# Optimization experiments

Measured on AMD Instinct MI355X. Metric: run time of the kernel, lower is better.

The kernel has to match this reference:

```python
import jax, jax.numpy as jnp
import numpy as np

H = 64  # hidden_size
B, T1, T2, T3 = 4096, 512, 256, 128


def setup_inputs() -> dict:
    key = jax.random.key(0)
    ks = jax.random.split(key, 18)
    s = 1.0 / np.sqrt(H)  # torch LSTMCell init scale
    def p(k, shape, scale):
        return jax.random.normal(k, shape, dtype=jnp.float32) * scale
    return {
        "x1": p(ks[0], (B, T1), 1.0),
        "x2": p(ks[1], (B, T2), 1.0),
        "x3": p(ks[2], (B, T3), 1.0),
        "W_ih3": p(ks[3], (4 * H, 3), s), "W_hh3": p(ks[4], (4 * H, H), s),
        "b_ih3": p(ks[5], (4 * H,), s), "b_hh3": p(ks[6], (4 * H,), s),
        "W_ih2": p(ks[7], (4 * H, 2), s), "W_hh2": p(ks[8], (4 * H, H), s),
        "b_ih2": p(ks[9], (4 * H,), s), "b_hh2": p(ks[10], (4 * H,), s),
        "W_ih1": p(ks[11], (4 * H, 1), s), "W_hh1": p(ks[12], (4 * H, H), s),
        "b_ih1": p(ks[13], (4 * H,), s), "b_hh1": p(ks[14], (4 * H,), s),
        "W_out": p(ks[15], (1, H), s), "b_out": p(ks[16], (1,), s),
    }


def reference(x1, x2, x3,
              W_ih3, W_hh3, b_ih3, b_hh3,
              W_ih2, W_hh2, b_ih2, b_hh2,
              W_ih1, W_hh1, b_ih1, b_hh1,
              W_out, b_out):
    h = W_hh3.shape[1]
    Bb, t1 = x1.shape
    r2, r3 = t1 // x2.shape[1], t1 // x3.shape[1]
    # Pad input weights to width 3; concat order is [x1, x2, x3] (zeros where absent),
    # so padded-column zeros reproduce the narrower cells exactly.
    Wi = jnp.stack([W_ih3,
                    jnp.pad(W_ih2, ((0, 0), (0, 1))),
                    jnp.pad(W_ih1, ((0, 0), (0, 2)))])  # [3, 4H, 3]
    Wh = jnp.stack([W_hh3, W_hh2, W_hh1])               # [3, 4H, H]
    bs = jnp.stack([b_ih3 + b_hh3, b_ih2 + b_hh2, b_ih1 + b_hh1])  # [3, 4H]
    t = np.arange(t1)
    has2 = (t % r2 == 0)
    has3 = (t % r3 == 0)
    assert not np.any(has3 & ~has2), "ratio2 must divide ratio3 for the concat-order mapping"
    # width 3 -> cell3 (type 0), width 2 -> cell2 (type 1), width 1 -> cell1 (type 2)
    step_type = jnp.asarray(2 - has2.astype(np.int32) - has3.astype(np.int32))
    xs = jnp.zeros((t1, Bb, 3), x1.dtype)
    xs = xs.at[:, :, 0].set(x1.T)
    xs = xs.at[::r2, :, 1].set(x2.T)
    xs = xs.at[::r3, :, 2].set(x3.T)

    def step(carry, inp):
        hx, cx = carry
        x, ty = inp
        g = x @ Wi[ty].T + hx @ Wh[ty].T + bs[ty]  # [B, 4H]
        i, f, gg, o = jnp.split(g, 4, axis=-1)     # torch gate order i,f,g,o
        cx = jax.nn.sigmoid(f) * cx + jax.nn.sigmoid(i) * jnp.tanh(gg)
        hx = jax.nn.sigmoid(o) * jnp.tanh(cx)
        return (hx, cx), None

    z = jnp.zeros((Bb, h), x1.dtype)
    (hx, _), _ = jax.lax.scan(step, (z, z), (xs, step_type))
    return jax.nn.sigmoid(hx @ W_out.T + b_out)  # [B, 1]
```

## Files before the change

### kernel.cpp

```cpp
#include <hip/hip_runtime.h>


typedef __attribute__((ext_vector_type(8))) short short8v;
typedef __attribute__((ext_vector_type(4))) float float4v;
typedef __attribute__((ext_vector_type(4))) unsigned short ushort4v;
typedef __attribute__((ext_vector_type(2))) unsigned int uint2v;

template <int N> struct IC { static constexpr int value = N; };

#define AST 72
#define XS1 516
#define XS2 260
#define XS3 132

#if __has_builtin(__builtin_amdgcn_exp2f)
#define EXP2F(x) __builtin_amdgcn_exp2f(x)
#else
#define EXP2F(x) exp2f(x)
#endif
#if __has_builtin(__builtin_amdgcn_rcpf)
#define RCPF(x) __builtin_amdgcn_rcpf(x)
#else
#define RCPF(x) (1.0f / (x))
#endif

#define NL2E -1.4426950408889634f
#define NL2E2 -2.8853900817779268f

__device__ __forceinline__ short f2bf(float f) {
  union { float f; unsigned u; } v; v.f = f;
  unsigned r = v.u + 0x7FFFu + ((v.u >> 16) & 1u);
  return (short)(r >> 16);
}
__device__ __forceinline__ float bf2f(short h) {
  union { float f; unsigned u; } v;
  v.u = ((unsigned)(unsigned short)h) << 16;
  return v.f;
}
__device__ __forceinline__ unsigned cvt_pk_bf16(float lo, float hi) {
  unsigned r;
  asm("v_cvt_pk_bf16_f32 %0, %1, %2" : "=v"(r) : "v"(lo), "v"(hi));
  return r;
}
__device__ __forceinline__ float rcp1p(float y) {
  return RCPF(1.0f + EXP2F(y));
}
__device__ __forceinline__ float fsig(float x) { return rcp1p(x * NL2E); }
__device__ __forceinline__ float ftanh(float x) {
  return __builtin_fmaf(2.0f, rcp1p(x * NL2E2), -1.0f);
}

__global__ __launch_bounds__(256, 1) void mlstm_kernel(
    const float* __restrict__ x1, const float* __restrict__ x2,
    const float* __restrict__ x3,
    const float* __restrict__ Wi3, const float* __restrict__ Wh3,
    const float* __restrict__ bi3, const float* __restrict__ bh3,
    const float* __restrict__ Wi2, const float* __restrict__ Wh2,
    const float* __restrict__ bi2, const float* __restrict__ bh2,
    const float* __restrict__ Wi1, const float* __restrict__ Wh1,
    const float* __restrict__ bi1, const float* __restrict__ bh1,
    const float* __restrict__ Wout, const float* __restrict__ bout,
    float* __restrict__ out) {
  __shared__ __attribute__((aligned(16))) short Ab0[16 * AST];
  __shared__ __attribute__((aligned(16))) short Ab1[16 * AST];
  __shared__ __attribute__((aligned(16))) short x1b[16 * XS1];
  __shared__ __attribute__((aligned(16))) short x2b[16 * XS2];
  __shared__ __attribute__((aligned(16))) short x3b[16 * XS3];

  const int tid = threadIdx.x;
  const int w = tid >> 6;
  const int lane = tid & 63;
  const int q = lane >> 4;
  const int c = lane & 15;
  const int R0 = blockIdx.x << 4;

  for (int idx = tid; idx < 16 * 512; idx += 256) {
    int m = idx >> 9, t = idx & 511;
    x1b[m * XS1 + t] = f2bf(x1[(size_t)(R0 + m) * 512 + t]);
  }
  for (int idx = tid; idx < 16 * 256; idx += 256) {
    int m = idx >> 8, t = idx & 255;
    x2b[m * XS2 + t] = f2bf(x2[(size_t)(R0 + m) * 256 + t]);
  }
  for (int idx = tid; idx < 16 * 128; idx += 256) {
    int m = idx >> 7, t = idx & 127;
    x3b[m * XS3 + t] = f2bf(x3[(size_t)(R0 + m) * 128 + t]);
  }
  for (int idx = tid; idx < 16 * AST; idx += 256) {
    Ab0[idx] = 0;
    Ab1[idx] = 0;
  }

  short8v whs[3][4][2];
  short8v wix[3][4];
  float4v bias4[3][4];
  {
    const float* WhA[3] = {Wh3, Wh2, Wh1};
    const float* WiA[3] = {Wi3, Wi2, Wi1};
    const float* biA[3] = {bi3, bi2, bi1};
    const float* bhA[3] = {bh3, bh2, bh1};
    const int wdt[3] = {3, 2, 1};
#pragma unroll
    for (int ty = 0; ty < 3; ++ty) {
#pragma unroll
      for (int g = 0; g < 4; ++g) {
        const float sg = (g == 2) ? NL2E2 : NL2E;
        const int n = g * 64 + 16 * w + c;
#pragma unroll
        for (int kf = 0; kf < 2; ++kf) {
          short8v v;
#pragma unroll
          for (int j = 0; j < 8; ++j)
            v[j] = f2bf(sg * WhA[ty][n * 64 + kf * 32 + q * 8 + j]);
          whs[ty][g][kf] = v;
        }
        short8v v2 = {0, 0, 0, 0, 0, 0, 0, 0};
        if (q == 0) {
#pragma unroll
          for (int j = 0; j < 3; ++j)
            if (j < wdt[ty]) v2[j] = f2bf(sg * WiA[ty][n * wdt[ty] + j]);
        }
        wix[ty][g] = v2;
        float4v bv;
#pragma unroll
        for (int r = 0; r < 4; ++r) {
          const int nd = g * 64 + 16 * w + 4 * q + r;
          bv[r] = sg * (biA[ty][nd] + bhA[ty][nd]);
        }
        bias4[ty][g] = bv;
      }
    }
  }

  const int afo = c * AST + q * 8;
  const int hwo = c * AST + 16 * w + 4 * q;
  const int x1o = c * XS1;
  const int x2o = c * XS2;
  const int x3o = c * XS3;

  __syncthreads();

  float cx[4] = {0.f, 0.f, 0.f, 0.f};

  auto stepf = [&](auto tyc, auto sc, const short* rbuf, short* wbuf,
                   ushort4v xav, unsigned xbv, unsigned short xcv) {
    constexpr int TY = decltype(tyc)::value;
    constexpr int S = decltype(sc)::value;
    short x1s = (short)xav[S];
    short x2s = (short)((S < 2) ? (xbv & 0xFFFFu) : (xbv >> 16));
    short8v a2 = {x1s, x2s, (short)xcv, 0, 0, 0, 0, 0};
    short8v a0 = *(const short8v*)(rbuf + afo);
    short8v a1 = *(const short8v*)(rbuf + afo + 32);

    float4v acc[4];
#pragma unroll
    for (int g = 0; g < 4; ++g) {
      float4v z = bias4[TY][g];
      z = __builtin_amdgcn_mfma_f32_16x16x32_bf16(wix[TY][g], a2, z, 0, 0, 0);
      z = __builtin_amdgcn_mfma_f32_16x16x32_bf16(whs[TY][g][0], a0, z, 0, 0, 0);
      z = __builtin_amdgcn_mfma_f32_16x16x32_bf16(whs[TY][g][1], a1, z, 0, 0, 0);
      acc[g] = z;
    }

    float h[4];
#pragma unroll
    for (int r = 0; r < 4; ++r) {
      float si = rcp1p(acc[0][r]);
      float sf = rcp1p(acc[1][r]);
      float tg = __builtin_fmaf(2.0f, rcp1p(acc[2][r]), -1.0f);
      float so = rcp1p(acc[3][r]);
      float ncx = __builtin_fmaf(sf, cx[r], si * tg);
      cx[r] = ncx;
      h[r] = so * ftanh(ncx);
    }
    uint2v pk;
    pk[0] = cvt_pk_bf16(h[0], h[1]);
    pk[1] = cvt_pk_bf16(h[2], h[3]);
    *(uint2v*)(wbuf + hwo) = pk;
    __syncthreads();
  };

  ushort4v xa = *(const ushort4v*)(x1b + x1o);
  unsigned xb = *(const unsigned*)(x2b + x2o);
  unsigned short xc = (unsigned short)x3b[x3o];

  for (int t4 = 0; t4 < 512; t4 += 4) {
    ushort4v xav = xa;
    unsigned xbv = xb;
    unsigned short xcv = xc;
    stepf(IC<0>{}, IC<0>{}, Ab0, Ab1, xav, xbv, xcv);
    xa = *(const ushort4v*)(x1b + x1o + t4 + 4);
    xb = *(const unsigned*)(x2b + x2o + ((t4 + 4) >> 1));
    xc = (unsigned short)x3b[x3o + ((t4 + 4) >> 2)];
    stepf(IC<2>{}, IC<1>{}, Ab1, Ab0, xav, xbv, xcv);
    stepf(IC<1>{}, IC<2>{}, Ab0, Ab1, xav, xbv, xcv);
    stepf(IC<2>{}, IC<3>{}, Ab1, Ab0, xav, xbv, xcv);
  }

  if (tid < 16) {
    float s = bout[0];
    const short* hr = Ab0 + tid * AST;
#pragma unroll
    for (int k = 0; k < 64; ++k)
      s = __builtin_fmaf(bf2f(hr[k]), Wout[k], s);
    out[R0 + tid] = fsig(s);
  }
}

extern "C" void kernel_launch(void* const* d_in, const int* in_sizes, int n_in,
                              void* d_out, int out_size, void* d_ws,
                              size_t ws_size, hipStream_t stream) {
  const float* x1 = (const float*)d_in[0];
  const float* x2 = (const float*)d_in[1];
  const float* x3 = (const float*)d_in[2];
  const float* Wi3 = (const float*)d_in[3];
  const float* Wh3 = (const float*)d_in[4];
  const float* bi3 = (const float*)d_in[5];
  const float* bh3 = (const float*)d_in[6];
  const float* Wi2 = (const float*)d_in[7];
  const float* Wh2 = (const float*)d_in[8];
  const float* bi2 = (const float*)d_in[9];
  const float* bh2 = (const float*)d_in[10];
  const float* Wi1 = (const float*)d_in[11];
  const float* Wh1 = (const float*)d_in[12];
  const float* bi1 = (const float*)d_in[13];
  const float* bh1 = (const float*)d_in[14];
  const float* Wout = (const float*)d_in[15];
  const float* bout = (const float*)d_in[16];
  float* out = (float*)d_out;

  hipLaunchKernelGGL(mlstm_kernel, dim3(256), dim3(256), 0, stream,
                     x1, x2, x3, Wi3, Wh3, bi3, bh3, Wi2, Wh2, bi2, bh2,
                     Wi1, Wh1, bi1, bh1, Wout, bout, out);
}
```

Before: 307.5 us.

## Pack two batch tiles per block and stream inputs from global memory

Each block now runs 512 threads covering two independent 16-row batch tiles, giving 128 blocks instead of 256. The up-front staging of x1/x2/x3 into LDS as bf16 is removed. Inputs are instead prefetched from global memory once per 4-step group and converted to bf16 in registers. This removes the LDS prologue and shrinks LDS use. In exchange, each barrier now spans 8 waves holding two unrelated recurrences, only half as many CUs get a block, and launch_bounds(512,2) tightens the register budget for the weight fragments held in registers, which may cause spills.

```diff
diff --git a/kernel.cpp b/kernel.cpp
--- a/kernel.cpp
+++ b/kernel.cpp
@@ -3,15 +3,13 @@
 
 typedef __attribute__((ext_vector_type(8))) short short8v;
 typedef __attribute__((ext_vector_type(4))) float float4v;
+typedef __attribute__((ext_vector_type(2))) float float2v;
 typedef __attribute__((ext_vector_type(4))) unsigned short ushort4v;
 typedef __attribute__((ext_vector_type(2))) unsigned int uint2v;
 
 template <int N> struct IC { static constexpr int value = N; };
 
 #define AST 72
-#define XS1 516
-#define XS2 260
-#define XS3 132
 
 #if __has_builtin(__builtin_amdgcn_exp2f)
 #define EXP2F(x) __builtin_amdgcn_exp2f(x)
@@ -50,7 +48,7 @@
   return __builtin_fmaf(2.0f, rcp1p(x * NL2E2), -1.0f);
 }
 
-__global__ __launch_bounds__(256, 1) void mlstm_kernel(
+__global__ __launch_bounds__(512, 2) void mlstm_kernel(
     const float* __restrict__ x1, const float* __restrict__ x2,
     const float* __restrict__ x3,
     const float* __restrict__ Wi3, const float* __restrict__ Wh3,
@@ -61,34 +59,21 @@
     const float* __restrict__ bi1, const float* __restrict__ bh1,
     const float* __restrict__ Wout, const float* __restrict__ bout,
     float* __restrict__ out) {
-  __shared__ __attribute__((aligned(16))) short Ab0[16 * AST];
-  __shared__ __attribute__((aligned(16))) short Ab1[16 * AST];
-  __shared__ __attribute__((aligned(16))) short x1b[16 * XS1];
-  __shared__ __attribute__((aligned(16))) short x2b[16 * XS2];
-  __shared__ __attribute__((aligned(16))) short x3b[16 * XS3];
+  __shared__ __attribute__((aligned(16))) short Ab0[2][16 * AST];
+  __shared__ __attribute__((aligned(16))) short Ab1[2][16 * AST];
 
   const int tid = threadIdx.x;
-  const int w = tid >> 6;
+  const int sb = tid >> 8;
+  const int tid8 = tid & 255;
+  const int w = tid8 >> 6;
   const int lane = tid & 63;
   const int q = lane >> 4;
   const int c = lane & 15;
-  const int R0 = blockIdx.x << 4;
-
-  for (int idx = tid; idx < 16 * 512; idx += 256) {
-    int m = idx >> 9, t = idx & 511;
-    x1b[m * XS1 + t] = f2bf(x1[(size_t)(R0 + m) * 512 + t]);
-  }
-  for (int idx = tid; idx < 16 * 256; idx += 256) {
-    int m = idx >> 8, t = idx & 255;
-    x2b[m * XS2 + t] = f2bf(x2[(size_t)(R0 + m) * 256 + t]);
-  }
-  for (int idx = tid; idx < 16 * 128; idx += 256) {
-    int m = idx >> 7, t = idx & 127;
-    x3b[m * XS3 + t] = f2bf(x3[(size_t)(R0 + m) * 128 + t]);
-  }
-  for (int idx = tid; idx < 16 * AST; idx += 256) {
-    Ab0[idx] = 0;
-    Ab1[idx] = 0;
+  const int R0 = blockIdx.x * 32 + sb * 16;
+
+  for (int idx = tid8; idx < 16 * AST; idx += 256) {
+    Ab0[sb][idx] = 0;
+    Ab1[sb][idx] = 0;
   }
 
   short8v whs[3][4][2];
@@ -134,9 +119,14 @@
 
   const int afo = c * AST + q * 8;
   const int hwo = c * AST + 16 * w + 4 * q;
-  const int x1o = c * XS1;
-  const int x2o = c * XS2;
-  const int x3o = c * XS3;
+  const short* Ar0 = &Ab0[sb][0];
+  short* Aw0 = &Ab0[sb][0];
+  const short* Ar1 = &Ab1[sb][0];
+  short* Aw1 = &Ab1[sb][0];
+
+  const float* xr1 = x1 + (size_t)(R0 + c) * 512;
+  const float* xr2 = x2 + (size_t)(R0 + c) * 256;
+  const float* xr3 = x3 + (size_t)(R0 + c) * 128;
 
   __syncthreads();
 
@@ -180,30 +170,43 @@
     __syncthreads();
   };
 
-  ushort4v xa = *(const ushort4v*)(x1b + x1o);
-  unsigned xb = *(const unsigned*)(x2b + x2o);
-  unsigned short xc = (unsigned short)x3b[x3o];
+  float4v xf1 = *(const float4v*)(xr1);
+  float2v xf2 = *(const float2v*)(xr2);
+  float xf3 = xr3[0];
+  ushort4v xa;
+  xa[0] = (unsigned short)f2bf(xf1[0]);
+  xa[1] = (unsigned short)f2bf(xf1[1]);
+  xa[2] = (unsigned short)f2bf(xf1[2]);
+  xa[3] = (unsigned short)f2bf(xf1[3]);
+  unsigned xb = ((unsigned)(unsigned short)f2bf(xf2[1]) << 16) |
+                (unsigned)(unsigned short)f2bf(xf2[0]);
+  unsigned short xc = (unsigned short)f2bf(xf3);
 
   for (int t4 = 0; t4 < 512; t4 += 4) {
-    ushort4v xav = xa;
-    unsigned xbv = xb;
-    unsigned short xcv = xc;
-    stepf(IC<0>{}, IC<0>{}, Ab0, Ab1, xav, xbv, xcv);
-    xa = *(const ushort4v*)(x1b + x1o + t4 + 4);
-    xb = *(const unsigned*)(x2b + x2o + ((t4 + 4) >> 1));
-    xc = (unsigned short)x3b[x3o + ((t4 + 4) >> 2)];
-    stepf(IC<2>{}, IC<1>{}, Ab1, Ab0, xav, xbv, xcv);
-    stepf(IC<1>{}, IC<2>{}, Ab0, Ab1, xav, xbv, xcv);
-    stepf(IC<2>{}, IC<3>{}, Ab1, Ab0, xav, xbv, xcv);
-  }
-
-  if (tid < 16) {
+    stepf(IC<0>{}, IC<0>{}, Ar0, Aw1, xa, xb, xc);
+    int tp = (t4 + 4 > 508) ? 508 : (t4 + 4);
+    xf1 = *(const float4v*)(xr1 + tp);
+    xf2 = *(const float2v*)(xr2 + (tp >> 1));
+    xf3 = xr3[tp >> 2];
+    stepf(IC<2>{}, IC<1>{}, Ar1, Aw0, xa, xb, xc);
+    stepf(IC<1>{}, IC<2>{}, Ar0, Aw1, xa, xb, xc);
+    stepf(IC<2>{}, IC<3>{}, Ar1, Aw0, xa, xb, xc);
+    xa[0] = (unsigned short)f2bf(xf1[0]);
+    xa[1] = (unsigned short)f2bf(xf1[1]);
+    xa[2] = (unsigned short)f2bf(xf1[2]);
+    xa[3] = (unsigned short)f2bf(xf1[3]);
+    xb = ((unsigned)(unsigned short)f2bf(xf2[1]) << 16) |
+         (unsigned)(unsigned short)f2bf(xf2[0]);
+    xc = (unsigned short)f2bf(xf3);
+  }
+
+  if (tid8 < 16) {
     float s = bout[0];
-    const short* hr = Ab0 + tid * AST;
+    const short* hr = &Ab0[sb][0] + tid8 * AST;
 #pragma unroll
     for (int k = 0; k < 64; ++k)
       s = __builtin_fmaf(bf2f(hr[k]), Wout[k], s);
-    out[R0 + tid] = fsig(s);
+    out[R0 + tid8] = fsig(s);
   }
 }
 
@@ -229,7 +232,7 @@
   const float* bout = (const float*)d_in[16];
   float* out = (float*)d_out;
 
-  hipLaunchKernelGGL(mlstm_kernel, dim3(256), dim3(256), 0, stream,
+  hipLaunchKernelGGL(mlstm_kernel, dim3(128), dim3(512), 0, stream,
                      x1, x2, x3, Wi3, Wh3, bi3, bh3, Wi2, Wh2, bi2, bh2,
                      Wi1, Wh1, bi1, bh1, Wout, bout, out);
 }
```

After: 455.1 us. 1.48x slower.

## Stream inputs from global per step and fuse gate nonlinearities with fewer reciprocals

Applied to the files above, without the earlier changes.

Drops the upfront staging of all x1/x2/x3 sequences into LDS. Each thread now prefetches the next group of four timesteps straight from global memory during the step loop and packs them into bf16 with cvt_pk and byte-permute, which removes the prologue load and convert phase. The gate math is also restructured to share reciprocals: sigmoid(i)*tanh(g) and sigmoid(o)*tanh(c) each become a single reciprocal of a product of exp terms, with clamps added to avoid overflow. The cost is global-load latency inside the serial recurrence, hidden only by one group of prefetch.

```diff
diff --git a/kernel.cpp b/kernel.cpp
--- a/kernel.cpp
+++ b/kernel.cpp
@@ -3,15 +3,13 @@
 
 typedef __attribute__((ext_vector_type(8))) short short8v;
 typedef __attribute__((ext_vector_type(4))) float float4v;
-typedef __attribute__((ext_vector_type(4))) unsigned short ushort4v;
+typedef __attribute__((ext_vector_type(2))) float float2v;
+typedef __attribute__((ext_vector_type(4))) unsigned int uint4v;
 typedef __attribute__((ext_vector_type(2))) unsigned int uint2v;
 
 template <int N> struct IC { static constexpr int value = N; };
 
 #define AST 72
-#define XS1 516
-#define XS2 260
-#define XS3 132
 
 #if __has_builtin(__builtin_amdgcn_exp2f)
 #define EXP2F(x) __builtin_amdgcn_exp2f(x)
@@ -42,13 +40,21 @@
   asm("v_cvt_pk_bf16_f32 %0, %1, %2" : "=v"(r) : "v"(lo), "v"(hi));
   return r;
 }
+__device__ __forceinline__ unsigned permb(unsigned hi, unsigned lo, unsigned sel) {
+#if __has_builtin(__builtin_amdgcn_perm)
+  return __builtin_amdgcn_perm(hi, lo, sel);
+#else
+  union { unsigned u[2]; unsigned char b[8]; } s;
+  s.u[0] = lo; s.u[1] = hi;
+  unsigned r = 0;
+  for (int i = 0; i < 4; ++i) r |= (unsigned)s.b[(sel >> (8 * i)) & 7] << (8 * i);
+  return r;
+#endif
+}
 __device__ __forceinline__ float rcp1p(float y) {
   return RCPF(1.0f + EXP2F(y));
 }
 __device__ __forceinline__ float fsig(float x) { return rcp1p(x * NL2E); }
-__device__ __forceinline__ float ftanh(float x) {
-  return __builtin_fmaf(2.0f, rcp1p(x * NL2E2), -1.0f);
-}
 
 __global__ __launch_bounds__(256, 1) void mlstm_kernel(
     const float* __restrict__ x1, const float* __restrict__ x2,
@@ -63,9 +69,6 @@
     float* __restrict__ out) {
   __shared__ __attribute__((aligned(16))) short Ab0[16 * AST];
   __shared__ __attribute__((aligned(16))) short Ab1[16 * AST];
-  __shared__ __attribute__((aligned(16))) short x1b[16 * XS1];
-  __shared__ __attribute__((aligned(16))) short x2b[16 * XS2];
-  __shared__ __attribute__((aligned(16))) short x3b[16 * XS3];
 
   const int tid = threadIdx.x;
   const int w = tid >> 6;
@@ -74,22 +77,18 @@
   const int c = lane & 15;
   const int R0 = blockIdx.x << 4;
 
-  for (int idx = tid; idx < 16 * 512; idx += 256) {
-    int m = idx >> 9, t = idx & 511;
-    x1b[m * XS1 + t] = f2bf(x1[(size_t)(R0 + m) * 512 + t]);
-  }
-  for (int idx = tid; idx < 16 * 256; idx += 256) {
-    int m = idx >> 8, t = idx & 255;
-    x2b[m * XS2 + t] = f2bf(x2[(size_t)(R0 + m) * 256 + t]);
-  }
-  for (int idx = tid; idx < 16 * 128; idx += 256) {
-    int m = idx >> 7, t = idx & 127;
-    x3b[m * XS3 + t] = f2bf(x3[(size_t)(R0 + m) * 128 + t]);
-  }
   for (int idx = tid; idx < 16 * AST; idx += 256) {
     Ab0[idx] = 0;
     Ab1[idx] = 0;
   }
+
+  const float* xr1 = x1 + (size_t)(R0 + c) * 512;
+  const float* xr2 = x2 + (size_t)(R0 + c) * 256;
+  const float* xr3 = x3 + (size_t)(R0 + c) * 128;
+
+  float4v xf1 = *(const float4v*)(xr1);
+  float2v xf2 = *(const float2v*)(xr2);
+  float xf3 = xr3[0];
 
   short8v whs[3][4][2];
   short8v wix[3][4];
@@ -134,21 +133,29 @@
 
   const int afo = c * AST + q * 8;
   const int hwo = c * AST + 16 * w + 4 * q;
-  const int x1o = c * XS1;
-  const int x2o = c * XS2;
-  const int x3o = c * XS3;
 
   __syncthreads();
 
   float cx[4] = {0.f, 0.f, 0.f, 0.f};
 
-  auto stepf = [&](auto tyc, auto sc, const short* rbuf, short* wbuf,
-                   ushort4v xav, unsigned xbv, unsigned short xcv) {
+  unsigned d0, d1, d2, d3, xcw;
+  auto cvtgrp = [&]() {
+    unsigned pA = cvt_pk_bf16(xf1[0], xf1[1]);
+    unsigned pB = cvt_pk_bf16(xf1[2], xf1[3]);
+    unsigned p2 = cvt_pk_bf16(xf2[0], xf2[1]);
+    xcw = cvt_pk_bf16(xf3, 0.0f);
+    d0 = permb(p2, pA, 0x05040100);
+    d1 = permb(p2, pA, 0x05040302);
+    d2 = permb(p2, pB, 0x07060100);
+    d3 = permb(p2, pB, 0x07060302);
+  };
+  cvtgrp();
+
+  auto stepf = [&](auto tyc, unsigned dS, unsigned dx3, const short* rbuf,
+                   short* wbuf) {
     constexpr int TY = decltype(tyc)::value;
-    constexpr int S = decltype(sc)::value;
-    short x1s = (short)xav[S];
-    short x2s = (short)((S < 2) ? (xbv & 0xFFFFu) : (xbv >> 16));
-    short8v a2 = {x1s, x2s, (short)xcv, 0, 0, 0, 0, 0};
+    uint4v au = {dS, dx3, 0u, 0u};
+    short8v a2 = __builtin_bit_cast(short8v, au);
     short8v a0 = *(const short8v*)(rbuf + afo);
     short8v a1 = *(const short8v*)(rbuf + afo + 32);
 
@@ -165,13 +172,15 @@
     float h[4];
 #pragma unroll
     for (int r = 0; r < 4; ++r) {
-      float si = rcp1p(acc[0][r]);
-      float sf = rcp1p(acc[1][r]);
-      float tg = __builtin_fmaf(2.0f, rcp1p(acc[2][r]), -1.0f);
-      float so = rcp1p(acc[3][r]);
-      float ncx = __builtin_fmaf(sf, cx[r], si * tg);
+      float e0 = EXP2F(acc[0][r]);
+      float e1 = EXP2F(acc[1][r]);
+      float e2 = EXP2F(__builtin_fminf(acc[2][r], 60.0f));
+      float e3 = EXP2F(acc[3][r]);
+      float sitg = (1.0f - e2) * RCPF((1.0f + e0) * (1.0f + e2));
+      float ncx = __builtin_fmaf(RCPF(1.0f + e1), cx[r], sitg);
       cx[r] = ncx;
-      h[r] = so * ftanh(ncx);
+      float e4 = EXP2F(__builtin_fminf(ncx * NL2E2, 60.0f));
+      h[r] = (1.0f - e4) * RCPF((1.0f + e3) * (1.0f + e4));
     }
     uint2v pk;
     pk[0] = cvt_pk_bf16(h[0], h[1]);
@@ -180,21 +189,16 @@
     __syncthreads();
   };
 
-  ushort4v xa = *(const ushort4v*)(x1b + x1o);
-  unsigned xb = *(const unsigned*)(x2b + x2o);
-  unsigned short xc = (unsigned short)x3b[x3o];
-
   for (int t4 = 0; t4 < 512; t4 += 4) {
-    ushort4v xav = xa;
-    unsigned xbv = xb;
-    unsigned short xcv = xc;
-    stepf(IC<0>{}, IC<0>{}, Ab0, Ab1, xav, xbv, xcv);
-    xa = *(const ushort4v*)(x1b + x1o + t4 + 4);
-    xb = *(const unsigned*)(x2b + x2o + ((t4 + 4) >> 1));
-    xc = (unsigned short)x3b[x3o + ((t4 + 4) >> 2)];
-    stepf(IC<2>{}, IC<1>{}, Ab1, Ab0, xav, xbv, xcv);
-    stepf(IC<1>{}, IC<2>{}, Ab0, Ab1, xav, xbv, xcv);
-    stepf(IC<2>{}, IC<3>{}, Ab1, Ab0, xav, xbv, xcv);
+    stepf(IC<0>{}, d0, xcw, Ab0, Ab1);
+    int tp = (t4 + 4 > 508) ? 508 : (t4 + 4);
+    xf1 = *(const float4v*)(xr1 + tp);
+    xf2 = *(const float2v*)(xr2 + (tp >> 1));
+    xf3 = xr3[tp >> 2];
+    stepf(IC<2>{}, d1, xcw, Ab1, Ab0);
+    stepf(IC<1>{}, d2, xcw, Ab0, Ab1);
+    stepf(IC<2>{}, d3, xcw, Ab1, Ab0);
+    cvtgrp();
   }
 
   if (tid < 16) {
```

After: 347.0 us. 12.8% more time.
